# Kernel tuning notes

Measured on AMD Instinct MI355X. Metric: run time of the kernel, lower is better.

Reference implementation:

```python
import jax, jax.numpy as jnp
import numpy as np

DEPTH = 12  # perfect binary tree: 2**DEPTH - 1 internal nodes, 2**DEPTH leaf children


def setup_inputs() -> dict:
    key = jax.random.key(0)
    k0, k1, k2, k3, k4 = jax.random.split(key, 5)
    H = 1024   # hidden_size
    I = 1024   # input_size
    N = 2 ** DEPTH - 1  # internal nodes, heap order (root = 0)
    scale = 0.02  # keep gates out of saturation
    emb = jax.random.normal(k0, (N, I), jnp.float32)
    W_ih = jax.random.normal(k1, (8 * H, I), jnp.float32) * scale
    W_hh = jax.random.normal(k2, (8 * H, 2 * H), jnp.float32) * scale
    b_ih = jax.random.normal(k3, (8 * H,), jnp.float32) * scale
    b_hh = jax.random.normal(k4, (8 * H,), jnp.float32) * scale
    return {"emb": emb, "W_ih": W_ih, "W_hh": W_hh, "b_ih": b_ih, "b_hh": b_hh}


def reference(emb, W_ih, W_hh, b_ih, b_hh):
    # Batched-by-level Tree-LSTM over a perfect binary tree in heap order.
    # nn.LSTM hidden size is 2H; node state passed upward is the first H dims.
    H2 = W_hh.shape[1]          # 2 * hidden_size
    H = H2 // 2
    b = b_ih + b_hh
    # Leaves: hidden = cell = zeros((1, H)) per the module's base case.
    h = jnp.zeros((2 ** DEPTH, H), emb.dtype)
    c = jnp.zeros((2 ** DEPTH, H), emb.dtype)
    for k in range(DEPTH - 1, -1, -1):  # bottom-up over levels
        n = 2 ** k
        # cat((a.hidden, b.hidden), dim=1): children of node j are 2j, 2j+1
        h_cat = h.reshape(n, H2)
        c_cat = c.reshape(n, H2)
        x = emb[n - 1: 2 * n - 1]  # level-k embeddings (heap indices n-1 .. 2n-2)
        gates = x @ W_ih.T + h_cat @ W_hh.T + b  # (n, 8H)
        i_, f_, g_, o_ = jnp.split(gates, 4, axis=1)  # PyTorch gate order i,f,g,o
        c_new = jax.nn.sigmoid(f_) * c_cat + jax.nn.sigmoid(i_) * jnp.tanh(g_)
        h_new = jax.nn.sigmoid(o_) * jnp.tanh(c_new)
        h = h_new[:, :H]  # slice back to hidden_size, as the module does
        c = c_new[:, :H]
    # root hidden and cell, each (1, H)
    return jnp.concatenate([h, c], axis=1)
```

## Files before the change

kernel.cpp:

```cpp
#include <hip/hip_runtime.h>
#include <hip/hip_bf16.h>
#include <math.h>


#define TREE_DEPTH 12

typedef unsigned short u16;
typedef unsigned int u32;
typedef __attribute__((ext_vector_type(8))) short bf16x8;
typedef __attribute__((ext_vector_type(4))) float f32x4;
typedef __attribute__((ext_vector_type(8))) unsigned short u16x8;
typedef __attribute__((ext_vector_type(2))) unsigned int u32x2;

__device__ __forceinline__ void gload16(const void* g, void* l) {
    __builtin_amdgcn_global_load_lds(
        (const __attribute__((address_space(1))) u32*)g,
        (__attribute__((address_space(3))) u32*)l, 16, 0, 0);
}

__device__ __forceinline__ u16 f2bf(float f) {
    __hip_bfloat16 h = __float2bfloat16(f);
    return *reinterpret_cast<u16*>(&h);
}
__device__ __forceinline__ u16 f2h(float f) {
    _Float16 h = (_Float16)f;
    return *reinterpret_cast<u16*>(&h);
}
__device__ __forceinline__ float h2f(u16 u) {
    _Float16 h;
    *reinterpret_cast<u16*>(&h) = u;
    return (float)h;
}
__device__ __forceinline__ float fsig(float x) {
    return 1.0f / (1.0f + __expf(-x));
}
__device__ __forceinline__ float ftanh(float x) {
    return 1.0f - 2.0f / (1.0f + __expf(2.0f * x));
}

__global__ void prep(const float* __restrict__ Wih,
                     const float* __restrict__ Whh,
                     const float* __restrict__ emb,
                     const float* __restrict__ b_ih,
                     const float* __restrict__ b_hh,
                     u16* __restrict__ Wih_p, u16* __restrict__ Whh_p,
                     u16* __restrict__ xb, float* __restrict__ bge) {
    const int bid = blockIdx.x;
    if (bid < 12288) {
        const int b = bid & 4095;
        const int seg = bid >> 12;
        const int x = b & 7, t = b >> 3;
        const int e = ((t & 3) * 8 + x) * 128 + (t >> 2);
        const int g = (e >> 4) & 3;
        const int j = (e >> 6) * 16 + (e & 15);
        const int wr = g * 2048 + j;
        const int col = threadIdx.x * 4;
        f32x4 v;
        u16* dst;
        if (seg == 0) {
            v = __builtin_nontemporal_load(
                (const f32x4*)(Wih + (size_t)wr * 1024 + col));
            dst = Wih_p + (size_t)e * 1024 + col;
        } else {
            v = __builtin_nontemporal_load(
                (const f32x4*)(Whh + (size_t)wr * 2048 + (seg - 1) * 1024 + col));
            dst = Whh_p + (size_t)e * 2048 + (seg - 1) * 1024 + col;
        }
        u32x2 p;
        p[0] = (u32)f2bf(v[0]) | ((u32)f2bf(v[1]) << 16);
        p[1] = (u32)f2bf(v[2]) | ((u32)f2bf(v[3]) << 16);
        *reinterpret_cast<u32x2*>(dst) = p;
    } else if (bid < 16383) {
        size_t idx = ((size_t)(bid - 12288) * 256 + threadIdx.x) * 4;
        f32x4 v = __builtin_nontemporal_load((const f32x4*)(emb + idx));
        u32x2 p;
        p[0] = (u32)f2bf(v[0]) | ((u32)f2bf(v[1]) << 16);
        p[1] = (u32)f2bf(v[2]) | ((u32)f2bf(v[3]) << 16);
        *reinterpret_cast<u32x2*>(xb + idx) = p;
    } else {
        int e = (bid - 16383) * 256 + threadIdx.x;
        int g = (e >> 4) & 3;
        int j = (e >> 6) * 16 + (e & 15);
        int r = g * 2048 + j;
        bge[e] = b_ih[r] + b_hh[r];
    }
}

__global__ __launch_bounds__(256) void gemm_gx(
    const u16* __restrict__ xb, const u16* __restrict__ Wp,
    const float* __restrict__ bge, u16* __restrict__ GX,
    u16* __restrict__ hdst, float* __restrict__ cdst)
{
    __shared__ u16 smem[128 * 140];

    const int gx_ = gridDim.x;
    int b = blockIdx.x + gx_ * blockIdx.y;
    const int x = b & 7, t = b >> 3;
    const int ct = (t & 3) * 8 + x;
    const int mt = t >> 2;
    const int m0 = mt * 128, c0 = ct * 128;

    const int tid = threadIdx.x, lane = tid & 63, w = tid >> 6;
    const int wr = (w >> 1) * 64, wc = (w & 1) * 64;

    f32x4 acc[4][4];
    #pragma unroll
    for (int i = 0; i < 4; ++i)
        #pragma unroll
        for (int j = 0; j < 4; ++j)
            acc[i][j] = f32x4{0.f, 0.f, 0.f, 0.f};

    const u16* gp[8];
    u16* dl[8];
    #pragma unroll
    for (int i = 0; i < 8; ++i) {
        const int s = tid + i * 256;
        const int r = s >> 3;
        const int o = (s & 7) * 16;
        const int ke = (o ^ ((r & 7) << 4)) >> 1;
        gp[i] = (r < 128) ? xb + (size_t)(m0 + r) * 1024 + ke
                          : Wp + (size_t)(c0 + r - 128) * 1024 + ke;
        dl[i] = smem + s * 8;
    }

    const int fl = lane & 15;
    const int kunit = (lane >> 4) * 16;

    for (int k0 = 0; k0 < 1024; k0 += 64) {
        #pragma unroll
        for (int i = 0; i < 8; ++i) { gload16(gp[i], dl[i]); gp[i] += 64; }
        __syncthreads();
        #pragma unroll
        for (int ks = 0; ks < 2; ++ks) {
            bf16x8 a_[4], b_[4];
            #pragma unroll
            for (int i = 0; i < 4; ++i) {
                const int ar = wr + i * 16 + fl;
                const int byo = (ks * 64 + kunit) ^ ((ar & 7) << 4);
                a_[i] = *reinterpret_cast<const bf16x8*>(
                    reinterpret_cast<const char*>(smem + ar * 64) + byo);
            }
            #pragma unroll
            for (int j = 0; j < 4; ++j) {
                const int br = 128 + wc + j * 16 + fl;
                const int byo = (ks * 64 + kunit) ^ ((br & 7) << 4);
                b_[j] = *reinterpret_cast<const bf16x8*>(
                    reinterpret_cast<const char*>(smem + br * 64) + byo);
            }
            #pragma unroll
            for (int i = 0; i < 4; ++i)
                #pragma unroll
                for (int j = 0; j < 4; ++j)
                    acc[i][j] = __builtin_amdgcn_mfma_f32_16x16x32_bf16(
                        a_[i], b_[j], acc[i][j], 0, 0, 0);
        }
        __syncthreads();
    }

    const int rg = (lane >> 4) * 4;
    if (m0 < 2047) {
        #pragma unroll
        for (int i = 0; i < 4; ++i)
            #pragma unroll
            for (int j = 0; j < 4; ++j) {
                const float bv = bge[c0 + wc + j * 16 + fl];
                #pragma unroll
                for (int r = 0; r < 4; ++r)
                    smem[(wr + i * 16 + rg + r) * 140 + (wc + j * 16 + fl)] =
                        f2h(acc[i][j][r] + bv);
            }
        __syncthreads();
        const int row_ = tid >> 4, chunk = tid & 15;
        #pragma unroll
        for (int it = 0; it < 8; ++it) {
            const int row = it * 16 + row_;
            if (m0 + row < 2047) {
                u16x8 v = *reinterpret_cast<const u16x8*>(
                    &smem[row * 140 + chunk * 8]);
                __builtin_nontemporal_store(
                    v, (u16x8*)(GX + (size_t)(m0 + row) * 4096 + c0 + chunk * 8));
            }
        }
    }
    if (m0 + 127 >= 2047) {
        const int jj = ((c0 + wc) >> 6) * 16 + fl;
        const float bi  = bge[c0 + wc + fl];
        const float bgg = bge[c0 + wc + 32 + fl];
        const float bo  = bge[c0 + wc + 48 + fl];
        #pragma unroll
        for (int i = 0; i < 4; ++i) {
            #pragma unroll
            for (int r = 0; r < 4; ++r) {
                const int m = m0 + wr + i * 16 + rg + r;
                if (m < 2047 || m >= 4095) continue;
                const int mm = m - 2047;
                const float cn = fsig(acc[i][0][r] + bi) * ftanh(acc[i][2][r] + bgg);
                const float hn = fsig(acc[i][3][r] + bo) * ftanh(cn);
                hdst[(size_t)(mm >> 1) * 2048 + (mm & 1) * 1024 + jj] = f2bf(hn);
                if (!(mm & 1))
                    cdst[(size_t)(mm >> 1) * 1024 + jj] = cn;
            }
        }
    }
}

template <int MI, int MW, int NW, int KG>
__global__ __launch_bounds__(MW* NW* KG * 64) void fused_level(
    const u16* __restrict__ A, const u16* __restrict__ Wp,
    const u16* __restrict__ GXl, const float* __restrict__ cprev,
    u16* __restrict__ hnext, float* __restrict__ cnext,
    float* __restrict__ outp, int n)
{
    constexpr int BM = MI * 16 * MW;
    constexpr int BN = NW * 64;
    constexpr int S = MW * NW;
    constexpr int NFR = MI * 4;
    constexpr int RC = NFR > 8 ? 8 : NFR;
    constexpr int NP = NFR / RC;
    constexpr int ROWS = BM + BN;
    constexpr int SLOTS = ROWS * 4;
    constexpr int GT = S * 64;
    constexpr int NL = SLOTS / GT;
    static_assert(SLOTS % GT == 0, "slot mapping must be exact");
    constexpr int STG = KG * ROWS * 64;
    constexpr int REDB = (KG > 1) ? (KG - 1) * S * RC * 64 * 16 : 0;
    constexpr int SMEM = STG > REDB ? STG : REDB;
    __shared__ __align__(16) char smem[SMEM];

    const int gx_ = gridDim.x;
    int b = blockIdx.x + gx_ * blockIdx.y;
    const int x = b & 7;
    int t = b >> 3;
    int ct, mt;
    if constexpr (NW == 2) {
        ct = (t & 3) * 8 + x; mt = t >> 2;
    } else {
        const int lo = t & 1; t >>= 1;
        ct = ((t & 3) * 8 + x) * 2 + lo; mt = t >> 2;
    }
    const int m0 = mt * BM;
    const int c0 = ct * BN;

    const int tid = threadIdx.x;
    const int lane = tid & 63;
    const int w = tid >> 6;
    const int kg = w / S;
    const int slot = w % S;
    const int wm = slot / NW;
    const int wn = slot % NW;

    const int Kc = 2048 / KG;
    const int kbeg = kg * Kc;

    u16* buf = (u16*)smem + (size_t)kg * ROWS * 32;

    const int gtid = slot * 64 + lane;
    const u16* gp[NL];
    u16* dl[NL];
    #pragma unroll
    for (int i = 0; i < NL; ++i) {
        const int s = gtid + i * GT;
        const int row = s >> 2;
        const int kof = (s & 3) * 8;
        if (row < BM) {
            int ar = m0 + row;
            if (ar >= n) ar = n - 1;
            gp[i] = A + (size_t)ar * 2048 + kbeg + kof;
        } else {
            gp[i] = Wp + (size_t)(c0 + row - BM) * 2048 + kbeg + kof;
        }
        dl[i] = buf + s * 8;
    }

    f32x4 acc[MI][4];
    #pragma unroll
    for (int mi = 0; mi < MI; ++mi)
        #pragma unroll
        for (int f = 0; f < 4; ++f)
            acc[mi][f] = f32x4{0.f, 0.f, 0.f, 0.f};

    const int fl = lane & 15;
    const int kb = (lane >> 4) * 8;
    const int ar0 = wm * MI * 16;
    const int bc0 = BM;

    for (int k0 = 0; k0 < Kc; k0 += 32) {
        #pragma unroll
        for (int i = 0; i < NL; ++i) { gload16(gp[i], dl[i]); gp[i] += 32; }
        __syncthreads();
        bf16x8 a_[MI], b_[4];
        #pragma unroll
        for (int mi = 0; mi < MI; ++mi)
            a_[mi] = *reinterpret_cast<const bf16x8*>(
                buf + (ar0 + mi * 16 + fl) * 32 + kb);
        #pragma unroll
        for (int f = 0; f < 4; ++f)
            b_[f] = *reinterpret_cast<const bf16x8*>(
                buf + (bc0 + wn * 64 + f * 16 + fl) * 32 + kb);
        #pragma unroll
        for (int mi = 0; mi < MI; ++mi)
            #pragma unroll
            for (int f = 0; f < 4; ++f)
                acc[mi][f] = __builtin_amdgcn_mfma_f32_16x16x32_bf16(
                    a_[mi], b_[f], acc[mi][f], 0, 0, 0);
        __syncthreads();
    }

    if constexpr (KG > 1) {
        f32x4* red = reinterpret_cast<f32x4*>(smem);
        #pragma unroll
        for (int pass = 0; pass < NP; ++pass) {
            if (kg > 0) {
                #pragma unroll
                for (int f = 0; f < RC; ++f) {
                    const int fr = pass * RC + f;
                    red[(((kg - 1) * S + slot) * RC + f) * 64 + lane] =
                        acc[fr >> 2][fr & 3];
                }
            }
            __syncthreads();
            if (kg == 0) {
                #pragma unroll
                for (int q = 1; q < KG; ++q)
                    #pragma unroll
                    for (int f = 0; f < RC; ++f) {
                        const int fr = pass * RC + f;
                        f32x4 v = red[(((q - 1) * S + slot) * RC + f) * 64 + lane];
                        acc[fr >> 2][fr & 3][0] += v[0];
                        acc[fr >> 2][fr & 3][1] += v[1];
                        acc[fr >> 2][fr & 3][2] += v[2];
                        acc[fr >> 2][fr & 3][3] += v[3];
                    }
            }
            __syncthreads();
        }
    }

    if (kg != 0) return;
    const int j = ((c0 + wn * 64) >> 6) * 16 + fl;
    #pragma unroll
    for (int mi = 0; mi < MI; ++mi) {
        #pragma unroll
        for (int r = 0; r < 4; ++r) {
            const int m = m0 + wm * MI * 16 + mi * 16 + (lane >> 4) * 4 + r;
            if (m >= n) continue;
            const u16* gx = GXl + (size_t)m * 4096 + c0 + wn * 64 + fl;
            const float i_ = acc[mi][0][r] + h2f(__builtin_nontemporal_load(gx));
            const float f_ = acc[mi][1][r] + h2f(__builtin_nontemporal_load(gx + 16));
            const float g_ = acc[mi][2][r] + h2f(__builtin_nontemporal_load(gx + 32));
            const float o_ = acc[mi][3][r] + h2f(__builtin_nontemporal_load(gx + 48));
            const float cc = __builtin_nontemporal_load(cprev + (size_t)m * 1024 + j);
            const float cn = fsig(f_) * cc + fsig(i_) * ftanh(g_);
            const float hn = fsig(o_) * ftanh(cn);
            if (hnext)
                hnext[(size_t)(m >> 1) * 2048 + (m & 1) * 1024 + j] = f2bf(hn);
            if (!(m & 1))
                __builtin_nontemporal_store(cn, cnext + (size_t)(m >> 1) * 1024 + j);
            if (outp) { outp[j] = hn; outp[1024 + j] = cn; }
        }
    }
}

extern "C" void kernel_launch(void* const* d_in, const int* in_sizes, int n_in,
                              void* d_out, int out_size, void* d_ws, size_t ws_size,
                              hipStream_t stream) {
    const float* emb  = (const float*)d_in[0];
    const float* W_ih = (const float*)d_in[1];
    const float* W_hh = (const float*)d_in[2];
    const float* b_ih = (const float*)d_in[3];
    const float* b_hh = (const float*)d_in[4];
    float* out = (float*)d_out;

    char* p = (char*)d_ws;
    float* bge  = (float*)p;  p += 16384;
    u16* Wih_p  = (u16*)p;    p += (size_t)4096 * 1024 * 2;
    u16* Whh_p  = (u16*)p;    p += (size_t)4096 * 2048 * 2;
    u16* xb     = (u16*)p;    p += (size_t)4096 * 1024 * 2;
    u16* GX     = (u16*)p;    p += (size_t)4096 * 4096 * 2;
    u16* Hcat   = (u16*)p;    p += (size_t)4096 * 2048 * 2;
    float* cbA  = (float*)p;  p += (size_t)1024 * 1024 * 4;
    float* cbB  = (float*)p;  p += (size_t)1024 * 1024 * 4;

    prep<<<16399, 256, 0, stream>>>(W_ih, W_hh, emb, b_ih, b_hh,
                                    Wih_p, Whh_p, xb, bge);

    #define OFF(k) (4096 - (2 << (k)))

    gemm_gx<<<dim3(32, 32), 256, 0, stream>>>(
        xb, Wih_p, bge, GX, Hcat + (size_t)OFF(10) * 2048, cbA);

    const float* cprev = cbA;
    float* cbufs[2] = {cbB, cbA};
    int t = 0;
    for (int k = TREE_DEPTH - 2; k >= 0; --k) {
        const int n = 1 << k;
        const u16* A = Hcat + (size_t)OFF(k) * 2048;
        const u16* GXl = GX + (size_t)(n - 1) * 4096;
        u16* hnext = (k > 0) ? (Hcat + (size_t)OFF(k - 1) * 2048) : nullptr;
        float* cnext = cbufs[t];
        float* outp = (k == 0) ? out : nullptr;

        if (k == 10) {
            fused_level<4, 1, 2, 2><<<dim3(16, 32), 256, 0, stream>>>(
                A, Whh_p, GXl, cprev, hnext, cnext, outp, n);
        } else if (k == 9) {
            fused_level<2, 1, 2, 2><<<dim3(16, 32), 256, 0, stream>>>(
                A, Whh_p, GXl, cprev, hnext, cnext, outp, n);
        } else if (k == 8) {
            fused_level<1, 1, 1, 4><<<dim3(16, 64), 256, 0, stream>>>(
                A, Whh_p, GXl, cprev, hnext, cnext, outp, n);
        } else {
            const int gx = (n >= 16) ? n / 16 : 1;
            fused_level<1, 1, 1, 8><<<dim3(gx, 64), 512, 0, stream>>>(
                A, Whh_p, GXl, cprev, hnext, cnext, outp, n);
        }
        cprev = cnext; t ^= 1;
    }
}
```

Before: 259.8 us.

## Double K-tile depth to 64 with XOR-swizzled LDS layout

Each main-loop iteration now stages 64 K-elements per row in LDS instead of 32, which halves the number of barrier pairs per tile. The 16-byte chunks within each 128-byte row are stored under an XOR swizzle keyed by the row index, so that MFMA operand reads from LDS spread across banks. The trade-off is twice the LDS staging footprint per block, which can reduce occupancy, plus more address arithmetic per load.

```diff
diff --git a/kernel.cpp b/kernel.cpp
--- a/kernel.cpp
+++ b/kernel.cpp
@@ -218,11 +218,11 @@
     constexpr int RC = NFR > 8 ? 8 : NFR;
     constexpr int NP = NFR / RC;
     constexpr int ROWS = BM + BN;
-    constexpr int SLOTS = ROWS * 4;
+    constexpr int SLOTS = ROWS * 8;
     constexpr int GT = S * 64;
     constexpr int NL = SLOTS / GT;
     static_assert(SLOTS % GT == 0, "slot mapping must be exact");
-    constexpr int STG = KG * ROWS * 64;
+    constexpr int STG = KG * ROWS * 128;
     constexpr int REDB = (KG > 1) ? (KG - 1) * S * RC * 64 * 16 : 0;
     constexpr int SMEM = STG > REDB ? STG : REDB;
     __shared__ __align__(16) char smem[SMEM];
@@ -252,7 +252,7 @@
     const int Kc = 2048 / KG;
     const int kbeg = kg * Kc;
 
-    u16* buf = (u16*)smem + (size_t)kg * ROWS * 32;
+    u16* buf = (u16*)smem + (size_t)kg * ROWS * 64;
 
     const int gtid = slot * 64 + lane;
     const u16* gp[NL];
@@ -260,14 +260,15 @@
     #pragma unroll
     for (int i = 0; i < NL; ++i) {
         const int s = gtid + i * GT;
-        const int row = s >> 2;
-        const int kof = (s & 3) * 8;
-        if (row < BM) {
-            int ar = m0 + row;
+        const int r = s >> 3;
+        const int o = (s & 7) * 16;
+        const int ke = (o ^ ((r & 7) << 4)) >> 1;
+        if (r < BM) {
+            int ar = m0 + r;
             if (ar >= n) ar = n - 1;
-            gp[i] = A + (size_t)ar * 2048 + kbeg + kof;
+            gp[i] = A + (size_t)ar * 2048 + kbeg + ke;
         } else {
-            gp[i] = Wp + (size_t)(c0 + row - BM) * 2048 + kbeg + kof;
+            gp[i] = Wp + (size_t)(c0 + r - BM) * 2048 + kbeg + ke;
         }
         dl[i] = buf + s * 8;
     }
@@ -280,29 +281,38 @@
             acc[mi][f] = f32x4{0.f, 0.f, 0.f, 0.f};
 
     const int fl = lane & 15;
-    const int kb = (lane >> 4) * 8;
+    const int kunit = (lane >> 4) * 16;
     const int ar0 = wm * MI * 16;
     const int bc0 = BM;
 
-    for (int k0 = 0; k0 < Kc; k0 += 32) {
-        #pragma unroll
-        for (int i = 0; i < NL; ++i) { gload16(gp[i], dl[i]); gp[i] += 32; }
+    for (int k0 = 0; k0 < Kc; k0 += 64) {
+        #pragma unroll
+        for (int i = 0; i < NL; ++i) { gload16(gp[i], dl[i]); gp[i] += 64; }
         __syncthreads();
-        bf16x8 a_[MI], b_[4];
-        #pragma unroll
-        for (int mi = 0; mi < MI; ++mi)
-            a_[mi] = *reinterpret_cast<const bf16x8*>(
-                buf + (ar0 + mi * 16 + fl) * 32 + kb);
-        #pragma unroll
-        for (int f = 0; f < 4; ++f)
-            b_[f] = *reinterpret_cast<const bf16x8*>(
-                buf + (bc0 + wn * 64 + f * 16 + fl) * 32 + kb);
-        #pragma unroll
-        for (int mi = 0; mi < MI; ++mi)
-            #pragma unroll
-            for (int f = 0; f < 4; ++f)
-                acc[mi][f] = __builtin_amdgcn_mfma_f32_16x16x32_bf16(
-                    a_[mi], b_[f], acc[mi][f], 0, 0, 0);
+        #pragma unroll
+        for (int ks = 0; ks < 2; ++ks) {
+            bf16x8 a_[MI], b_[4];
+            #pragma unroll
+            for (int mi = 0; mi < MI; ++mi) {
+                const int ar = ar0 + mi * 16 + fl;
+                const int byo = (ks * 64 + kunit) ^ ((ar & 7) << 4);
+                a_[mi] = *reinterpret_cast<const bf16x8*>(
+                    reinterpret_cast<const char*>(buf + ar * 64) + byo);
+            }
+            #pragma unroll
+            for (int f = 0; f < 4; ++f) {
+                const int br = bc0 + wn * 64 + f * 16 + fl;
+                const int byo = (ks * 64 + kunit) ^ ((br & 7) << 4);
+                b_[f] = *reinterpret_cast<const bf16x8*>(
+                    reinterpret_cast<const char*>(buf + br * 64) + byo);
+            }
+            #pragma unroll
+            for (int mi = 0; mi < MI; ++mi)
+                #pragma unroll
+                for (int f = 0; f < 4; ++f)
+                    acc[mi][f] = __builtin_amdgcn_mfma_f32_16x16x32_bf16(
+                        a_[mi], b_[f], acc[mi][f], 0, 0, 0);
+        }
         __syncthreads();
     }
 
```

Measured after the change: 221.0 us (median of 2 runs). -14.9%, faster.
